# Performance work log

Measured on AMD Instinct MI355X. Metric: run time of the kernel, lower is better.

Reference implementation:

```python
import jax, jax.numpy as jnp
import numpy as np

B, C, N = 32, 128, 64
HID = 2 * C
STEEPNESS = 50.0


def _bitonic_layers(n):
    """Index pairs (a, b) for each compare-exchange layer of a bitonic sorting
    network, matching diffsort's bitonic_network construction."""
    num_blocks = int(np.log2(n))
    assert n == 2 ** num_blocks
    layers = []
    for block in range(num_blocks):
        for layer in range(block + 1):
            m = 2 ** (block - layer)
            a_idx, b_idx = [], []
            for i in range(0, n, 2 * m):
                for j in range(m):
                    ix = i + j
                    a, b = ix, ix + m
                    # alternate direction within bitonic blocks
                    if (ix // 2 ** (block + 1)) % 2 == 1:
                        a, b = b, a
                    a_idx.append(a)
                    b_idx.append(b)
            layers.append((np.asarray(a_idx), np.asarray(b_idx)))
    return layers

_LAYERS = _bitonic_layers(N)  # 21 layers for N=64


def _diff_sort(scores):
    """Differentiable bitonic sort (diffsort, distribution='cauchy').
    Returns (soft-sorted scores, soft permutation matrix P) with
    sorted = scores @ P; the module applies P via bmm(P, rows)."""
    b, n = scores.shape
    x = scores
    P = jnp.broadcast_to(jnp.eye(n, dtype=scores.dtype), (b, n, n))
    inv_pi = 1.0 / np.pi
    for a_idx, b_idx in _LAYERS:
        xa, xb = x[:, a_idx], x[:, b_idx]
        alpha = jnp.arctan((xb - xa) * STEEPNESS) * inv_pi + 0.5  # Cauchy CDF
        x = x.at[:, a_idx].set(alpha * xa + (1.0 - alpha) * xb)
        x = x.at[:, b_idx].set((1.0 - alpha) * xa + alpha * xb)
        Pa, Pb = P[:, :, a_idx], P[:, :, b_idx]
        al = alpha[:, None, :]
        P = P.at[:, :, a_idx].set(al * Pa + (1.0 - al) * Pb)
        P = P.at[:, :, b_idx].set((1.0 - al) * Pa + al * Pb)
    return x, P


def setup_inputs() -> dict:
    key = jax.random.key(0)
    ks = jax.random.split(key, 9)
    s = 0.05  # keep score magnitudes reasonable under steepness=50
    return {
        "x": jax.random.normal(ks[0], (B, C, N, N), jnp.float32),
        "w1": jax.random.normal(ks[1], (HID, C), jnp.float32) * s,
        "b1": jax.random.normal(ks[2], (HID,), jnp.float32) * s,
        "w2": jax.random.normal(ks[3], (HID, HID), jnp.float32) * s,
        "b2": jax.random.normal(ks[4], (HID,), jnp.float32) * s,
        "w_row": jax.random.normal(ks[5], (HID, N), jnp.float32) * s,
        "b_row": jax.random.normal(ks[6], (1,), jnp.float32) * s,
        "w_col": jax.random.normal(ks[7], (HID, N), jnp.float32) * s,
        "b_col": jax.random.normal(ks[8], (1,), jnp.float32) * s,
    }


def reference(x, w1, b1, w2, b2, w_row, b_row, w_col, b_col):
    # feat_extractor: two 1x1 convs (pointwise channel GEMMs) + ReLU
    h = jax.nn.relu(jnp.einsum('bchw,oc->bohw', x, w1) + b1[None, :, None, None])
    h = jax.nn.relu(jnp.einsum('bchw,oc->bohw', h, w2) + b2[None, :, None, None])

    # row branch: Conv1d(HID*N,1,1) over flattened (channel, width) per row
    row_scores = jnp.einsum('bchw,cw->bh', h, w_row) + b_row  # (B, N)
    _, p_row = _diff_sort(row_scores)
    x = jnp.einsum('bij,bcjk->bcik', p_row, x)  # bmm(P_row, x) per channel

    # col branch: Conv1d(HID*N,1,1) over flattened (channel, height) per column
    col_scores = jnp.einsum('bchw,ch->bw', h, w_col) + b_col  # (B, N)
    _, p_col = _diff_sort(col_scores)
    # original: bmm(P_col, x^T) then view as (B,C,N,N) with NO transpose back
    x = jnp.einsum('bij,bckj->bcik', p_col, x)
    return x
```

## Files before the change

### kernel.cpp

```cpp
#include <hip/hip_runtime.h>
#include <math.h>

#define B_    32
#define C_    128
#define N_    64
#define HID_  256
#define PIX_  4096
#define STEEP 50.0f
#define INV_PI 0.318309886183790671f
#define LDH   272
#define LDX   72

typedef unsigned short u16;
typedef __attribute__((ext_vector_type(8))) short bf16x8;
typedef __attribute__((ext_vector_type(4))) float f32x4;

__device__ __forceinline__ u16 f2bf(float f) {
    unsigned int u = __builtin_bit_cast(unsigned int, f);
    unsigned int r = (u + 0x7FFFu + ((u >> 16) & 1u)) >> 16;
    return (u16)r;
}
__device__ __forceinline__ float bf2f(u16 h) {
    unsigned int u = ((unsigned int)h) << 16;
    return __builtin_bit_cast(float, u);
}
__device__ __forceinline__ int h1_idx(int p, int k) {
    return p * LDH + (((k >> 3) + (p & 7)) & 31) * 8 + (k & 7);
}
__device__ __forceinline__ int x_idx(int p, int k) {
    return p * LDH + 128 + (((k >> 3) + (p & 7)) & 15) * 8 + (k & 7);
}

__global__ void k0_init(float* __restrict__ col_s, const float* __restrict__ b_col) {
    int i = blockIdx.x * 256 + threadIdx.x;
    if (i < B_ * N_) col_s[i] = b_col[0];
}

__global__ void k_prep(const float* __restrict__ w1, const float* __restrict__ w2,
                       u16* __restrict__ w1h, u16* __restrict__ w1l,
                       u16* __restrict__ w2h, u16* __restrict__ w2l) {
    int i = blockIdx.x * 256 + threadIdx.x;
    if (i < HID_ * C_) {
        float v = w1[i];
        u16 h = f2bf(v);
        w1h[i] = h;
        w1l[i] = f2bf(v - bf2f(h));
    } else {
        int j = i - HID_ * C_;
        if (j < HID_ * HID_) {
            float v = w2[j];
            u16 h = f2bf(v);
            w2h[j] = h;
            w2l[j] = f2bf(v - bf2f(h));
        }
    }
}

__global__ __launch_bounds__(256) void k12_fused(
    const float* __restrict__ x,
    const u16* __restrict__ w1h, const u16* __restrict__ w1l,
    const float* __restrict__ b1,
    const u16* __restrict__ w2h, const u16* __restrict__ w2l,
    const float* __restrict__ b2, const float* __restrict__ w_row,
    const float* __restrict__ b_row, const float* __restrict__ w_col,
    float* __restrict__ row_s, float* __restrict__ col_s) {
    __shared__ __align__(16) u16 Lh[64 * LDH];
    __shared__ __align__(16) u16 Ll[64 * LDH];
    __shared__ float col_red[64];
    __shared__ float row_red;

    const int t = threadIdx.x;
    const int l = t & 63, w = t >> 6;
    const int col = l & 15, q = l >> 4;
    const int hrow = blockIdx.x;
    const int b = blockIdx.y;
    const float* xb = x + (size_t)b * C_ * PIX_ + hrow * 64;

    if (t < 64) col_red[t] = 0.f;
    if (t == 0) row_red = 0.f;

    {
        const int pt = t & 15, ct = t >> 4;
#pragma unroll
        for (int cc = 0; cc < 4; cc++) {
            const int c = cc * 32 + 2 * ct;
            float4 v0 = *(const float4*)&xb[(size_t)c * PIX_ + pt * 4];
            float4 v1 = *(const float4*)&xb[(size_t)(c + 1) * PIX_ + pt * 4];
            float a0[4] = {v0.x, v0.y, v0.z, v0.w};
            float a1[4] = {v1.x, v1.y, v1.z, v1.w};
#pragma unroll
            for (int j = 0; j < 4; j++) {
                int p = pt * 4 + j;
                u16 h0 = f2bf(a0[j]), h1v = f2bf(a1[j]);
                u16 l0 = f2bf(a0[j] - bf2f(h0)), l1 = f2bf(a1[j] - bf2f(h1v));
                int idx = x_idx(p, c);
                *(unsigned int*)&Lh[idx] = (unsigned int)h0 | ((unsigned int)h1v << 16);
                *(unsigned int*)&Ll[idx] = (unsigned int)l0 | ((unsigned int)l1 << 16);
            }
        }
    }
    __syncthreads();

    f32x4 acc[4][4];
#pragma unroll
    for (int i = 0; i < 4; i++)
#pragma unroll
        for (int j = 0; j < 4; j++) acc[i][j] = (f32x4){0.f, 0.f, 0.f, 0.f};

    bf16x8 ah[4], al_[4];
#pragma unroll
    for (int mf = 0; mf < 4; mf++) {
        size_t ro = (size_t)(64 * w + 16 * mf + col) * C_ + q * 8;
        ah[mf] = *(const bf16x8*)&w1h[ro];
        al_[mf] = *(const bf16x8*)&w1l[ro];
    }
#pragma unroll
    for (int kc = 0; kc < 4; kc++) {
        bf16x8 bh[4], bl[4];
#pragma unroll
        for (int nt = 0; nt < 4; nt++) {
            int idx = x_idx(nt * 16 + col, kc * 32 + q * 8);
            bh[nt] = *(const bf16x8*)&Lh[idx];
            bl[nt] = *(const bf16x8*)&Ll[idx];
        }
        bf16x8 ahn[4], aln[4];
        const int kn = (kc + 1) & 3;
#pragma unroll
        for (int mf = 0; mf < 4; mf++) {
            size_t ro = (size_t)(64 * w + 16 * mf + col) * C_ + kn * 32 + q * 8;
            ahn[mf] = *(const bf16x8*)&w1h[ro];
            aln[mf] = *(const bf16x8*)&w1l[ro];
        }
#pragma unroll
        for (int mf = 0; mf < 4; mf++)
#pragma unroll
            for (int nt = 0; nt < 4; nt++) {
                acc[mf][nt] = __builtin_amdgcn_mfma_f32_16x16x32_bf16(ah[mf], bh[nt], acc[mf][nt], 0, 0, 0);
                acc[mf][nt] = __builtin_amdgcn_mfma_f32_16x16x32_bf16(ah[mf], bl[nt], acc[mf][nt], 0, 0, 0);
                acc[mf][nt] = __builtin_amdgcn_mfma_f32_16x16x32_bf16(al_[mf], bh[nt], acc[mf][nt], 0, 0, 0);
            }
#pragma unroll
        for (int mf = 0; mf < 4; mf++) { ah[mf] = ahn[mf]; al_[mf] = aln[mf]; }
    }

    bf16x8 ah2[4], al2[4];
#pragma unroll
    for (int mf = 0; mf < 4; mf++) {
        size_t ro = (size_t)(64 * w + 16 * mf + col) * HID_ + q * 8;
        ah2[mf] = *(const bf16x8*)&w2h[ro];
        al2[mf] = *(const bf16x8*)&w2l[ro];
    }
    __syncthreads();

#pragma unroll
    for (int mf = 0; mf < 4; mf++) {
        int o = 64 * w + 16 * mf + q * 4;
        float bias[4];
#pragma unroll
        for (int r = 0; r < 4; r++) bias[r] = b1[o + r];
#pragma unroll
        for (int nt = 0; nt < 4; nt++) {
            int p = nt * 16 + col;
            u16 hh[4], ll[4];
#pragma unroll
            for (int r = 0; r < 4; r++) {
                float v = fmaxf(acc[mf][nt][r] + bias[r], 0.f);
                u16 h = f2bf(v);
                hh[r] = h;
                ll[r] = f2bf(v - bf2f(h));
            }
            int idx = h1_idx(p, o);
            *(unsigned long long*)&Lh[idx] =
                (unsigned long long)hh[0] | ((unsigned long long)hh[1] << 16) |
                ((unsigned long long)hh[2] << 32) | ((unsigned long long)hh[3] << 48);
            *(unsigned long long*)&Ll[idx] =
                (unsigned long long)ll[0] | ((unsigned long long)ll[1] << 16) |
                ((unsigned long long)ll[2] << 32) | ((unsigned long long)ll[3] << 48);
        }
    }
    __syncthreads();

    f32x4 acc2[4][4];
#pragma unroll
    for (int i = 0; i < 4; i++)
#pragma unroll
        for (int j = 0; j < 4; j++) acc2[i][j] = (f32x4){0.f, 0.f, 0.f, 0.f};

#pragma unroll
    for (int kc = 0; kc < 8; kc++) {
        bf16x8 bh[4], bl[4];
#pragma unroll
        for (int nt = 0; nt < 4; nt++) {
            int idx = h1_idx(nt * 16 + col, kc * 32 + q * 8);
            bh[nt] = *(const bf16x8*)&Lh[idx];
            bl[nt] = *(const bf16x8*)&Ll[idx];
        }
        bf16x8 ahn[4], aln[4];
        const int kn = (kc + 1) & 7;
#pragma unroll
        for (int mf = 0; mf < 4; mf++) {
            size_t ro = (size_t)(64 * w + 16 * mf + col) * HID_ + kn * 32 + q * 8;
            ahn[mf] = *(const bf16x8*)&w2h[ro];
            aln[mf] = *(const bf16x8*)&w2l[ro];
        }
#pragma unroll
        for (int mf = 0; mf < 4; mf++)
#pragma unroll
            for (int nt = 0; nt < 4; nt++) {
                acc2[mf][nt] = __builtin_amdgcn_mfma_f32_16x16x32_bf16(ah2[mf], bh[nt], acc2[mf][nt], 0, 0, 0);
                acc2[mf][nt] = __builtin_amdgcn_mfma_f32_16x16x32_bf16(ah2[mf], bl[nt], acc2[mf][nt], 0, 0, 0);
                acc2[mf][nt] = __builtin_amdgcn_mfma_f32_16x16x32_bf16(al2[mf], bh[nt], acc2[mf][nt], 0, 0, 0);
            }
#pragma unroll
        for (int mf = 0; mf < 4; mf++) { ah2[mf] = ahn[mf]; al2[mf] = aln[mf]; }
    }

    float rpart = 0.f;
    float cpart[4] = {0.f, 0.f, 0.f, 0.f};
#pragma unroll
    for (int mf = 0; mf < 4; mf++) {
        int o = 64 * w + 16 * mf + q * 4;
#pragma unroll
        for (int r = 0; r < 4; r++) {
            float bias = b2[o + r];
            float wcv = w_col[(o + r) * N_ + hrow];
#pragma unroll
            for (int nt = 0; nt < 4; nt++) {
                int wc = nt * 16 + col;
                float v = fmaxf(acc2[mf][nt][r] + bias, 0.f);
                rpart += v * w_row[(o + r) * N_ + wc];
                cpart[nt] += v * wcv;
            }
        }
    }
#pragma unroll
    for (int off = 32; off; off >>= 1) rpart += __shfl_xor(rpart, off, 64);
    if (l == 0) atomicAdd(&row_red, rpart);
#pragma unroll
    for (int nt = 0; nt < 4; nt++) {
        float cp = cpart[nt];
        cp += __shfl_xor(cp, 16, 64);
        cp += __shfl_xor(cp, 32, 64);
        if (l < 16) atomicAdd(&col_red[nt * 16 + l], cp);
    }
    __syncthreads();
    if (t < 64) atomicAdd(&col_s[b * N_ + t], col_red[t]);
    if (t == 0) row_s[b * N_ + hrow] = b_row[0] + row_red;
}

__global__ __launch_bounds__(256) void k4_diffsort(const float* __restrict__ row_s,
                                                   const float* __restrict__ col_s,
                                                   u16* __restrict__ prow_h, u16* __restrict__ prow_l,
                                                   u16* __restrict__ pcol_h, u16* __restrict__ pcol_l) {
    __shared__ float Ps[64 * 65];
    __shared__ float xs[64];
    __shared__ float als[32];
    const int t = threadIdx.x;
    const int which = blockIdx.x & 1;
    const int b = blockIdx.x >> 1;
    const float* sc = which ? col_s : row_s;
    u16* Ph = which ? pcol_h : prow_h;
    u16* Pl = which ? pcol_l : prow_l;

    if (t < 64) xs[t] = sc[b * 64 + t];
#pragma unroll
    for (int k = 0; k < 16; k++) {
        int idx = t + k * 256;
        int i = idx >> 6, j = idx & 63;
        Ps[i * 65 + j] = (i == j) ? 1.f : 0.f;
    }
    __syncthreads();

    const int r = t & 63, pg = t >> 6;
    for (int bl = 0; bl < 6; bl++) {
        for (int ly = 0; ly <= bl; ly++) {
            int sh = bl - ly;
            int m = 1 << sh;
            if (t < 32) {
                int i = (t >> sh) << (sh + 1);
                int j = t & (m - 1);
                int ix = i + j;
                int a = ix, bi = ix + m;
                if ((ix >> (bl + 1)) & 1) { int tmp = a; a = bi; bi = tmp; }
                float xa = xs[a], xbv = xs[bi];
                float al = atanf((xbv - xa) * STEEP) * INV_PI + 0.5f;
                als[t] = al;
                xs[a] = al * xa + (1.f - al) * xbv;
                xs[bi] = (1.f - al) * xa + al * xbv;
            }
            __syncthreads();
#pragma unroll
            for (int pi = 0; pi < 8; pi++) {
                int p = pg * 8 + pi;
                int i = (p >> sh) << (sh + 1);
                int j = p & (m - 1);
                int ix = i + j;
                int a = ix, bi = ix + m;
                if ((ix >> (bl + 1)) & 1) { int tmp = a; a = bi; bi = tmp; }
                float al = als[p];
                float Pa = Ps[r * 65 + a], Pb = Ps[r * 65 + bi];
                Ps[r * 65 + a] = al * Pa + (1.f - al) * Pb;
                Ps[r * 65 + bi] = (1.f - al) * Pa + al * Pb;
            }
            __syncthreads();
        }
    }
#pragma unroll
    for (int k = 0; k < 16; k++) {
        int idx = t + k * 256;
        int i = idx >> 6, j = idx & 63;
        float v = Ps[i * 65 + j];
        u16 h = f2bf(v);
        Ph[b * 4096 + idx] = h;
        Pl[b * 4096 + idx] = f2bf(v - bf2f(h));
    }
}

__global__ __launch_bounds__(256) void k5_permute(const float* __restrict__ x,
                                                  const u16* __restrict__ pcol_h,
                                                  const u16* __restrict__ pcol_l,
                                                  const u16* __restrict__ prow_h,
                                                  const u16* __restrict__ prow_l,
                                                  float* __restrict__ out) {
    __shared__ __align__(16) u16 Xh[64 * LDX];
    __shared__ __align__(16) u16 Xl[64 * LDX];
    __shared__ __align__(16) u16 Zh[64 * LDX];
    __shared__ __align__(16) u16 Zl[64 * LDX];
    const int t = threadIdx.x;
    const int l = t & 63, w = t >> 6;
    const int col = l & 15, q = l >> 4;
    const int b = blockIdx.y;
    const int cbase = blockIdx.x * 4;
    const int i0 = w * 16;

    const u16* pch = pcol_h + (size_t)b * 4096;
    const u16* pcl = pcol_l + (size_t)b * 4096;
    const u16* prh = prow_h + (size_t)b * 4096;
    const u16* prl = prow_l + (size_t)b * 4096;

    bf16x8 pcA_h[2], pcA_l[2];
#pragma unroll
    for (int ks = 0; ks < 2; ks++) {
        pcA_h[ks] = *(const bf16x8*)&pch[(i0 + col) * 64 + q * 8 + ks * 32];
        pcA_l[ks] = *(const bf16x8*)&pcl[(i0 + col) * 64 + q * 8 + ks * 32];
    }

    for (int ci = 0; ci < 4; ci++) {
        const int c = cbase + ci;
        const float* xc = x + ((size_t)b * C_ + c) * PIX_;
#pragma unroll
        for (int k = 0; k < 4; k++) {
            int f = t + k * 256;
            int rw = f >> 4, c4 = f & 15;
            float4 v = *(const float4*)&xc[f * 4];
            u16 h0 = f2bf(v.x), h1 = f2bf(v.y), h2 = f2bf(v.z), h3 = f2bf(v.w);
            ushort4 hv = {h0, h1, h2, h3};
            ushort4 lv = {f2bf(v.x - bf2f(h0)), f2bf(v.y - bf2f(h1)),
                          f2bf(v.z - bf2f(h2)), f2bf(v.w - bf2f(h3))};
            *(ushort4*)&Xh[rw * LDX + c4 * 4] = hv;
            *(ushort4*)&Xl[rw * LDX + c4 * 4] = lv;
        }
        __syncthreads();

        f32x4 acc[4];
#pragma unroll
        for (int nt = 0; nt < 4; nt++) acc[nt] = (f32x4){0.f, 0.f, 0.f, 0.f};
#pragma unroll
        for (int ks = 0; ks < 2; ks++) {
            bf16x8 ah = pcA_h[ks], al_ = pcA_l[ks];
#pragma unroll
            for (int nt = 0; nt < 4; nt++) {
                bf16x8 bh = *(const bf16x8*)&Xh[(nt * 16 + col) * LDX + q * 8 + ks * 32];
                bf16x8 bl = *(const bf16x8*)&Xl[(nt * 16 + col) * LDX + q * 8 + ks * 32];
                acc[nt] = __builtin_amdgcn_mfma_f32_16x16x32_bf16(ah, bh, acc[nt], 0, 0, 0);
                acc[nt] = __builtin_amdgcn_mfma_f32_16x16x32_bf16(ah, bl, acc[nt], 0, 0, 0);
                acc[nt] = __builtin_amdgcn_mfma_f32_16x16x32_bf16(al_, bh, acc[nt], 0, 0, 0);
            }
        }
#pragma unroll
        for (int nt = 0; nt < 4; nt++)
#pragma unroll
            for (int r = 0; r < 4; r++) {
                float v = acc[nt][r];
                u16 h = f2bf(v);
                int rw = i0 + q * 4 + r;
                Zh[rw * LDX + nt * 16 + col] = h;
                Zl[rw * LDX + nt * 16 + col] = f2bf(v - bf2f(h));
            }

        f32x4 acc2[4];
#pragma unroll
        for (int nt = 0; nt < 4; nt++) acc2[nt] = (f32x4){0.f, 0.f, 0.f, 0.f};
#pragma unroll
        for (int ks = 0; ks < 2; ks++) {
            bf16x8 ah = *(const bf16x8*)&Zh[(i0 + col) * LDX + q * 8 + ks * 32];
            bf16x8 al_ = *(const bf16x8*)&Zl[(i0 + col) * LDX + q * 8 + ks * 32];
#pragma unroll
            for (int nt = 0; nt < 4; nt++) {
                bf16x8 bh = *(const bf16x8*)&prh[(nt * 16 + col) * 64 + q * 8 + ks * 32];
                bf16x8 bl = *(const bf16x8*)&prl[(nt * 16 + col) * 64 + q * 8 + ks * 32];
                acc2[nt] = __builtin_amdgcn_mfma_f32_16x16x32_bf16(ah, bh, acc2[nt], 0, 0, 0);
                acc2[nt] = __builtin_amdgcn_mfma_f32_16x16x32_bf16(ah, bl, acc2[nt], 0, 0, 0);
                acc2[nt] = __builtin_amdgcn_mfma_f32_16x16x32_bf16(al_, bh, acc2[nt], 0, 0, 0);
            }
        }
        float* oc = out + ((size_t)b * C_ + c) * PIX_;
#pragma unroll
        for (int nt = 0; nt < 4; nt++)
#pragma unroll
            for (int r = 0; r < 4; r++)
                oc[(i0 + q * 4 + r) * 64 + nt * 16 + col] = acc2[nt][r];
        __syncthreads();
    }
}

extern "C" void kernel_launch(void* const* d_in, const int* in_sizes, int n_in,
                              void* d_out, int out_size, void* d_ws, size_t ws_size,
                              hipStream_t stream) {
    const float* x = (const float*)d_in[0];
    const float* w1 = (const float*)d_in[1];
    const float* b1 = (const float*)d_in[2];
    const float* w2 = (const float*)d_in[3];
    const float* b2 = (const float*)d_in[4];
    const float* w_row = (const float*)d_in[5];
    const float* b_row = (const float*)d_in[6];
    const float* w_col = (const float*)d_in[7];
    const float* b_col = (const float*)d_in[8];
    float* out = (float*)d_out;

    char* ws = (char*)d_ws;
    u16* w1h = (u16*)(ws);
    u16* w1l = (u16*)(ws + 65536);
    u16* w2h = (u16*)(ws + 131072);
    u16* w2l = (u16*)(ws + 262144);
    float* row_s = (float*)(ws + 393216);
    float* col_s = (float*)(ws + 401408);
    u16* prow_h = (u16*)(ws + 409600);
    u16* prow_l = (u16*)(ws + 671744);
    u16* pcol_h = (u16*)(ws + 933888);
    u16* pcol_l = (u16*)(ws + 1196032);

    hipLaunchKernelGGL(k0_init, dim3(8), dim3(256), 0, stream, col_s, b_col);
    hipLaunchKernelGGL(k_prep, dim3(384), dim3(256), 0, stream, w1, w2, w1h, w1l, w2h, w2l);
    hipLaunchKernelGGL(k12_fused, dim3(64, 32), dim3(256), 0, stream,
                       x, w1h, w1l, b1, w2h, w2l, b2, w_row, b_row, w_col, row_s, col_s);
    hipLaunchKernelGGL(k4_diffsort, dim3(64), dim3(256), 0, stream,
                       row_s, col_s, prow_h, prow_l, pcol_h, pcol_l);
    hipLaunchKernelGGL(k5_permute, dim3(32, 32), dim3(256), 0, stream,
                       x, pcol_h, pcol_l, prow_h, prow_l, out);
}
```

Before: 292.2 us.

## Register-resident diffsort with shuffles, prefetch x in permute, merge init into prep

The diffsort kernel now keeps the score vector and permutation matrix in registers, one column per lane and 16 rows per wave, and does the compare-exchange with cross-lane xor shuffles. This removes the shared-memory traffic and the two block barriers per layer. The permute kernel prefetches the next channel's x tile into registers while computing the current one, and the col_s init kernel is folded into the weight-prep kernel to save a launch. Each lane now computes atan redundantly, and the register use for the prefetch buffer rises.

```diff
diff --git a/kernel.cpp b/kernel.cpp
--- a/kernel.cpp
+++ b/kernel.cpp
@@ -31,15 +31,12 @@
     return p * LDH + 128 + (((k >> 3) + (p & 7)) & 15) * 8 + (k & 7);
 }
 
-__global__ void k0_init(float* __restrict__ col_s, const float* __restrict__ b_col) {
+__global__ void k_prep(const float* __restrict__ w1, const float* __restrict__ w2,
+                       u16* __restrict__ w1h, u16* __restrict__ w1l,
+                       u16* __restrict__ w2h, u16* __restrict__ w2l,
+                       float* __restrict__ col_s, const float* __restrict__ b_col) {
     int i = blockIdx.x * 256 + threadIdx.x;
     if (i < B_ * N_) col_s[i] = b_col[0];
-}
-
-__global__ void k_prep(const float* __restrict__ w1, const float* __restrict__ w2,
-                       u16* __restrict__ w1h, u16* __restrict__ w1l,
-                       u16* __restrict__ w2h, u16* __restrict__ w2l) {
-    int i = blockIdx.x * 256 + threadIdx.x;
     if (i < HID_ * C_) {
         float v = w1[i];
         u16 h = f2bf(v);
@@ -252,67 +249,45 @@
                                                    const float* __restrict__ col_s,
                                                    u16* __restrict__ prow_h, u16* __restrict__ prow_l,
                                                    u16* __restrict__ pcol_h, u16* __restrict__ pcol_l) {
-    __shared__ float Ps[64 * 65];
-    __shared__ float xs[64];
-    __shared__ float als[32];
     const int t = threadIdx.x;
+    const int lane = t & 63, w = t >> 6;
     const int which = blockIdx.x & 1;
     const int b = blockIdx.x >> 1;
     const float* sc = which ? col_s : row_s;
     u16* Ph = which ? pcol_h : prow_h;
     u16* Pl = which ? pcol_l : prow_l;
 
-    if (t < 64) xs[t] = sc[b * 64 + t];
-#pragma unroll
-    for (int k = 0; k < 16; k++) {
-        int idx = t + k * 256;
-        int i = idx >> 6, j = idx & 63;
-        Ps[i * 65 + j] = (i == j) ? 1.f : 0.f;
-    }
-    __syncthreads();
-
-    const int r = t & 63, pg = t >> 6;
+    float xv = sc[b * 64 + lane];
+    float P[16];
+#pragma unroll
+    for (int r = 0; r < 16; r++) P[r] = ((w * 16 + r) == lane) ? 1.f : 0.f;
+
+#pragma unroll
     for (int bl = 0; bl < 6; bl++) {
+#pragma unroll
         for (int ly = 0; ly <= bl; ly++) {
-            int sh = bl - ly;
-            int m = 1 << sh;
-            if (t < 32) {
-                int i = (t >> sh) << (sh + 1);
-                int j = t & (m - 1);
-                int ix = i + j;
-                int a = ix, bi = ix + m;
-                if ((ix >> (bl + 1)) & 1) { int tmp = a; a = bi; bi = tmp; }
-                float xa = xs[a], xbv = xs[bi];
-                float al = atanf((xbv - xa) * STEEP) * INV_PI + 0.5f;
-                als[t] = al;
-                xs[a] = al * xa + (1.f - al) * xbv;
-                xs[bi] = (1.f - al) * xa + al * xbv;
-            }
-            __syncthreads();
-#pragma unroll
-            for (int pi = 0; pi < 8; pi++) {
-                int p = pg * 8 + pi;
-                int i = (p >> sh) << (sh + 1);
-                int j = p & (m - 1);
-                int ix = i + j;
-                int a = ix, bi = ix + m;
-                if ((ix >> (bl + 1)) & 1) { int tmp = a; a = bi; bi = tmp; }
-                float al = als[p];
-                float Pa = Ps[r * 65 + a], Pb = Ps[r * 65 + bi];
-                Ps[r * 65 + a] = al * Pa + (1.f - al) * Pb;
-                Ps[r * 65 + bi] = (1.f - al) * Pa + al * Pb;
-            }
-            __syncthreads();
-        }
-    }
-#pragma unroll
-    for (int k = 0; k < 16; k++) {
-        int idx = t + k * 256;
-        int i = idx >> 6, j = idx & 63;
-        float v = Ps[i * 65 + j];
+            const int sh = bl - ly;
+            const int m = 1 << sh;
+            float xp = __shfl_xor(xv, m, 64);
+            int lower = ((lane >> sh) & 1) ^ 1;
+            int swp = (lane >> (bl + 1)) & 1;
+            float diff = (lower ^ swp) ? (xp - xv) : (xv - xp);
+            float al = atanf(diff * STEEP) * INV_PI + 0.5f;
+            xv = al * xv + (1.f - al) * xp;
+#pragma unroll
+            for (int r = 0; r < 16; r++) {
+                float Pp = __shfl_xor(P[r], m, 64);
+                P[r] = al * P[r] + (1.f - al) * Pp;
+            }
+        }
+    }
+#pragma unroll
+    for (int r = 0; r < 16; r++) {
+        float v = P[r];
         u16 h = f2bf(v);
-        Ph[b * 4096 + idx] = h;
-        Pl[b * 4096 + idx] = f2bf(v - bf2f(h));
+        int row = w * 16 + r;
+        Ph[(size_t)b * 4096 + row * 64 + lane] = h;
+        Pl[(size_t)b * 4096 + row * 64 + lane] = f2bf(v - bf2f(h));
     }
 }
 
@@ -345,14 +320,19 @@
         pcA_l[ks] = *(const bf16x8*)&pcl[(i0 + col) * 64 + q * 8 + ks * 32];
     }
 
+    float4 pv[4];
+    {
+        const float* xc0 = x + ((size_t)b * C_ + cbase) * PIX_;
+#pragma unroll
+        for (int k = 0; k < 4; k++) pv[k] = *(const float4*)&xc0[(t + k * 256) * 4];
+    }
+
     for (int ci = 0; ci < 4; ci++) {
-        const int c = cbase + ci;
-        const float* xc = x + ((size_t)b * C_ + c) * PIX_;
 #pragma unroll
         for (int k = 0; k < 4; k++) {
             int f = t + k * 256;
             int rw = f >> 4, c4 = f & 15;
-            float4 v = *(const float4*)&xc[f * 4];
+            float4 v = pv[k];
             u16 h0 = f2bf(v.x), h1 = f2bf(v.y), h2 = f2bf(v.z), h3 = f2bf(v.w);
             ushort4 hv = {h0, h1, h2, h3};
             ushort4 lv = {f2bf(v.x - bf2f(h0)), f2bf(v.y - bf2f(h1)),
@@ -362,6 +342,12 @@
         }
         __syncthreads();
 
+        if (ci < 3) {
+            const float* xcn = x + ((size_t)b * C_ + cbase + ci + 1) * PIX_;
+#pragma unroll
+            for (int k = 0; k < 4; k++) pv[k] = *(const float4*)&xcn[(t + k * 256) * 4];
+        }
+
         f32x4 acc[4];
 #pragma unroll
         for (int nt = 0; nt < 4; nt++) acc[nt] = (f32x4){0.f, 0.f, 0.f, 0.f};
@@ -404,7 +390,7 @@
                 acc2[nt] = __builtin_amdgcn_mfma_f32_16x16x32_bf16(al_, bh, acc2[nt], 0, 0, 0);
             }
         }
-        float* oc = out + ((size_t)b * C_ + c) * PIX_;
+        float* oc = out + ((size_t)b * C_ + cbase + ci) * PIX_;
 #pragma unroll
         for (int nt = 0; nt < 4; nt++)
 #pragma unroll
@@ -440,8 +426,8 @@
     u16* pcol_h = (u16*)(ws + 933888);
     u16* pcol_l = (u16*)(ws + 1196032);
 
-    hipLaunchKernelGGL(k0_init, dim3(8), dim3(256), 0, stream, col_s, b_col);
-    hipLaunchKernelGGL(k_prep, dim3(384), dim3(256), 0, stream, w1, w2, w1h, w1l, w2h, w2l);
+    hipLaunchKernelGGL(k_prep, dim3(384), dim3(256), 0, stream, w1, w2, w1h, w1l, w2h, w2l,
+                       col_s, b_col);
     hipLaunchKernelGGL(k12_fused, dim3(64, 32), dim3(256), 0, stream,
                        x, w1h, w1l, b1, w2h, w2l, b2, w_row, b_row, w_col, row_s, col_s);
     hipLaunchKernelGGL(k4_diffsort, dim3(64), dim3(256), 0, stream,
```

Result: faster. 275.9 us (-5.6%).
